# Kernel optimization log

Hardware: AMD Instinct MI355X
Metric: run time of the kernel (lower is better)

## Reference

```python
import jax, jax.numpy as jnp
import numpy as np

B, N, D, OUT = 8, 2048, 128, 128


def setup_inputs() -> dict:
    key = jax.random.key(0)
    k1, k2, kk, kv, ko, kb = jax.random.split(key, 6)
    x1 = jax.random.normal(k1, (B, N, D), dtype=jnp.float32)
    x2 = jax.random.normal(k2, (B, N, D), dtype=jnp.float32)
    # torch Linear weight layout: [out_features, in_features]; xavier_normal std
    std_k = np.sqrt(2.0 / (D + D))
    Wk = jax.random.normal(kk, (D, D), dtype=jnp.float32) * std_k
    Wv = jax.random.normal(kv, (D, D), dtype=jnp.float32) * std_k
    std_o = np.sqrt(1.0 / D)
    Wo = jax.random.uniform(ko, (OUT, D), dtype=jnp.float32, minval=-std_o, maxval=std_o)
    bo = jax.random.uniform(kb, (OUT,), dtype=jnp.float32, minval=-std_o, maxval=std_o)
    return {"x1": x1, "x2": x2, "Wk": Wk, "Wv": Wv, "Wo": Wo, "bo": bo}


def reference(x1, x2, Wk, Wv, Wo, bo):
    # key projections (no bias)
    h1 = jnp.einsum('bnd,kd->bnk', x1, Wk)  # [B,N1,D]
    h2 = jnp.einsum('bmd,kd->bmk', x2, Wk)  # [B,N2,D]
    e12 = jnp.einsum('bnk,bmk->bnm', h1, h2)  # [B,N1,N2]
    e21 = jnp.einsum('bmk,bnk->bmn', h2, h1)  # [B,N2,N1]
    # NOTE: original uses Softmax(dim=1), i.e. over the QUERY axis — faithful here.
    a12 = jax.nn.softmax(e12, axis=1)
    a21 = jax.nn.softmax(e21, axis=1)
    v2 = jnp.einsum('bmd,kd->bmk', x2, Wv)
    v1 = jnp.einsum('bnd,kd->bnk', x1, Wv)
    n12 = jnp.einsum('bnm,bmk->bnk', a12, v2)  # [B,N1,D]
    n21 = jnp.einsum('bmn,bnk->bmk', a21, v1)  # [B,N2,D]
    msg1 = jax.nn.leaky_relu(jnp.einsum('bnk,ok->bno', n12, Wo) + bo, 0.01)
    msg2 = jax.nn.leaky_relu(jnp.einsum('bmk,ok->bmo', n21, Wo) + bo, 0.01)
    return (msg1, msg2)
```

## Files before the change

### kernel.cpp

```cpp
#include <hip/hip_runtime.h>
#include <hip/hip_bf16.h>

#define B_ 8
#define N_ 2048
#define D_ 128
#define CFIX 95.0f

typedef __attribute__((ext_vector_type(8))) _Float16 half8;
typedef __attribute__((ext_vector_type(8))) unsigned short ushort8;
typedef __attribute__((ext_vector_type(4))) float floatx4;
typedef __attribute__((ext_vector_type(16))) float floatx16;

__device__ __forceinline__ unsigned short f2h(float f) {
    _Float16 h = (_Float16)f;
    union { _Float16 h; unsigned short u; } v; v.h = h;
    return v.u;
}
__device__ __forceinline__ ushort4 f2h4(float4 f) {
    ushort4 u; u.x = f2h(f.x); u.y = f2h(f.y); u.z = f2h(f.z); u.w = f2h(f.w);
    return u;
}
__device__ __forceinline__ half8 mk_half8(unsigned int a, unsigned int b,
                                          unsigned int c, unsigned int d) {
    union { unsigned int u[4]; half8 h; } v;
    v.u[0] = a; v.u[1] = b; v.u[2] = c; v.u[3] = d;
    return v.h;
}
__device__ __forceinline__ void plswap(unsigned int &x, unsigned int &y, int hi) {
    unsigned int sx = (unsigned int)__shfl_xor((int)x, 32, 64);
    unsigned int sy = (unsigned int)__shfl_xor((int)y, 32, 64);
    x = hi ? sy : x;
    y = hi ? y : sx;
}

__global__ __launch_bounds__(256)
void proj_kernel(const float* __restrict__ x1, const float* __restrict__ x2,
                 const float* __restrict__ Wk, const float* __restrict__ Wv,
                 unsigned short* __restrict__ h1, unsigned short* __restrict__ h2,
                 unsigned short* __restrict__ v1t, unsigned short* __restrict__ v2t,
                 float* __restrict__ sums)
{
    __shared__ unsigned short Xs[64][136];
    __shared__ unsigned short Ws[128][136];
    const int which = blockIdx.y;
    const float* x = (which & 1) ? x2 : x1;
    const float* W = (which & 2) ? Wv : Wk;
    const int rowbase = blockIdx.x * 64;
    const int t = threadIdx.x;

    {
        int base = (blockIdx.y * 256 + blockIdx.x) * 32;
        if (t < 32) sums[base + t] = 0.0f;
    }

    for (int it = 0; it < 8; ++it) {
        int idx = t + 256 * it;
        int r = idx >> 5, c = (idx & 31) * 4;
        float4 f = *(const float4*)(x + (size_t)(rowbase + r) * 128 + c);
        *(ushort4*)&Xs[r][c] = f2h4(f);
    }
    for (int it = 0; it < 16; ++it) {
        int idx = t + 256 * it;
        int r = idx >> 5, c = (idx & 31) * 4;
        float4 f = *(const float4*)(W + (size_t)r * 128 + c);
        *(ushort4*)&Ws[r][c] = f2h4(f);
    }
    __syncthreads();

    const int lane = t & 63, wave = t >> 6, l15 = lane & 15, quad = lane >> 4;
    half8 a[4];
    for (int ks = 0; ks < 4; ++ks)
        a[ks] = *(const half8*)&Xs[wave * 16 + l15][ks * 32 + quad * 8];
    __syncthreads();

    if (which < 2) {
        unsigned short* out = which ? h2 : h1;
        for (int c = 0; c < 8; ++c) {
            floatx4 acc = {0.f, 0.f, 0.f, 0.f};
            for (int ks = 0; ks < 4; ++ks) {
                half8 b = *(const half8*)&Ws[c * 16 + l15][ks * 32 + quad * 8];
                acc = __builtin_amdgcn_mfma_f32_16x16x32_f16(a[ks], b, acc, 0, 0, 0);
            }
            int col = c * 16 + l15;
            for (int r = 0; r < 4; ++r)
                Xs[wave * 16 + quad * 4 + r][col] = f2h(acc[r]);
        }
        __syncthreads();
        for (int i = 0; i < 4; ++i) {
            int idx = t + 256 * i;
            int r = idx >> 4, c8 = idx & 15;
            ushort8 v = *(const ushort8*)&Xs[r][c8 * 8];
            *(ushort8*)(out + (size_t)(rowbase + r) * 128 + c8 * 8) = v;
        }
    } else {
        unsigned short* vt = (which == 2) ? v1t : v2t;
        unsigned short (*Xt)[68] = (unsigned short (*)[68])&Xs[0][0];
        for (int c = 0; c < 8; ++c) {
            floatx4 acc = {0.f, 0.f, 0.f, 0.f};
            for (int ks = 0; ks < 4; ++ks) {
                half8 b = *(const half8*)&Ws[c * 16 + l15][ks * 32 + quad * 8];
                acc = __builtin_amdgcn_mfma_f32_16x16x32_f16(a[ks], b, acc, 0, 0, 0);
            }
            int col = c * 16 + l15;
            for (int r = 0; r < 4; ++r)
                Xt[col][wave * 16 + quad * 4 + r] = f2h(acc[r]);
        }
        __syncthreads();
        const int bb = rowbase >> 11;
        const int n0 = rowbase & (N_ - 1);
        for (int i = 0; i < 8; ++i) {
            int idx = t + 256 * i;
            int d = idx >> 4, q4 = idx & 15;
            ushort4 v = *(const ushort4*)&Xt[d][q4 * 4];
            *(ushort4*)(vt + ((size_t)bb * 128 + d) * N_ + n0 + q4 * 4) = v;
        }
    }
}

__global__ __launch_bounds__(512, 2)
void stats_kernel(const unsigned short* __restrict__ h1g, const unsigned short* __restrict__ h2g,
                  float* __restrict__ rsum, float* __restrict__ csum)
{
    __shared__ __align__(16) unsigned short Ks[2][2][64][136];

    const int bid = blockIdx.x;
    const int b = bid & 7;
    const int qblk = (bid >> 3) & 15;
    const int dir = bid >> 7;
    const int qbase = qblk * 128;

    const unsigned short* Q = (dir ? h2g : h1g) + (size_t)b * N_ * 128;
    const unsigned short* K = (dir ? h1g : h2g) + (size_t)b * N_ * 128;
    float* outp = (dir ? csum : rsum) + (size_t)b * N_;

    const int t = threadIdx.x;
    const int lane = t & 63, wave = t >> 6;
    const int l31 = lane & 31, h = lane >> 5;
    const int qt = wave & 3, j = wave >> 2;

    half8 qf[8];
    #pragma unroll
    for (int ds = 0; ds < 8; ++ds)
        qf[ds] = *(const half8*)(Q + (size_t)(qbase + qt * 32 + l31) * 128 + ds * 16 + h * 8);

    int krow[2], kc8[2];
    #pragma unroll
    for (int s2 = 0; s2 < 2; ++s2) {
        int idx = t + 512 * s2;
        krow[s2] = idx >> 4; kc8[s2] = idx & 15;
    }
    half8 kreg[2][2];
    #pragma unroll
    for (int jj = 0; jj < 2; ++jj)
        #pragma unroll
        for (int s2 = 0; s2 < 2; ++s2)
            kreg[jj][s2] = *(const half8*)(K + (size_t)(jj * 1024 + krow[s2]) * 128 + kc8[s2] * 8);
    #pragma unroll
    for (int jj = 0; jj < 2; ++jj)
        #pragma unroll
        for (int s2 = 0; s2 < 2; ++s2)
            *(half8*)&Ks[0][jj][krow[s2]][kc8[s2] * 8] = kreg[jj][s2];
    #pragma unroll
    for (int jj = 0; jj < 2; ++jj)
        #pragma unroll
        for (int s2 = 0; s2 < 2; ++s2)
            kreg[jj][s2] = *(const half8*)(K + (size_t)(jj * 1024 + 64 + krow[s2]) * 128 + kc8[s2] * 8);
    __syncthreads();

    float racc = 0.0f;

    for (int kt = 0; kt < 16; ++kt) {
        const int cb = kt & 1;
        #pragma unroll
        for (int jj = 0; jj < 2; ++jj)
            #pragma unroll
            for (int s2 = 0; s2 < 2; ++s2)
                *(half8*)&Ks[cb ^ 1][jj][krow[s2]][kc8[s2] * 8] = kreg[jj][s2];
        int ktp = (kt + 2 < 16) ? kt + 2 : 15;
        #pragma unroll
        for (int jj = 0; jj < 2; ++jj)
            #pragma unroll
            for (int s2 = 0; s2 < 2; ++s2)
                kreg[jj][s2] = *(const half8*)(K + (size_t)(jj * 1024 + ktp * 64 + krow[s2]) * 128 + kc8[s2] * 8);

        #pragma unroll
        for (int ks = 0; ks < 2; ++ks) {
            floatx16 acc;
            #pragma unroll
            for (int r = 0; r < 16; ++r) acc[r] = -CFIX;
            #pragma unroll
            for (int ds = 0; ds < 8; ++ds) {
                half8 kf = *(const half8*)&Ks[cb][j][ks * 32 + l31][ds * 16 + h * 8];
                acc = __builtin_amdgcn_mfma_f32_32x32x16_f16(kf, qf[ds], acc, 0, 0, 0);
            }
            float e[16];
            #pragma unroll
            for (int r = 0; r < 16; ++r) e[r] = __expf(acc[r]);
            #pragma unroll
            for (int st = 8; st > 0; st >>= 1)
                #pragma unroll
                for (int r = 0; r < st; ++r) e[r] += e[r + st];
            racc += e[0];
        }
        __syncthreads();
    }

    racc += __shfl_xor(racc, 32, 64);
    if (h == 0)
        atomicAdd(&outp[qbase + qt * 32 + l31], racc);
}

__global__ __launch_bounds__(512)
void log_kernel(float* __restrict__ sums, const float* __restrict__ Wo,
                unsigned short* __restrict__ wo16)
{
    int i = blockIdx.x * 1024 + threadIdx.x * 2;
    float2 v = *(float2*)(sums + i);
    v.x = -(CFIX + __logf(v.x));
    v.y = -(CFIX + __logf(v.y));
    *(float2*)(sums + i) = v;
    if (blockIdx.x < 16) {
        float2 w = *(const float2*)(Wo + i);
        unsigned int pk = (unsigned int)f2h(w.x) | ((unsigned int)f2h(w.y) << 16);
        *(unsigned int*)(wo16 + i) = pk;
    }
}

__global__ __launch_bounds__(512, 2)
void attn_kernel(const unsigned short* __restrict__ h1g, const unsigned short* __restrict__ h2g,
                 const unsigned short* __restrict__ v1tg, const unsigned short* __restrict__ v2tg,
                 const float* __restrict__ rsumL, const float* __restrict__ csumL,
                 const unsigned short* __restrict__ wo16, const float* __restrict__ bo,
                 float* __restrict__ outp, int zbase)
{
    __shared__ __align__(16) unsigned short Ks[2][2][64][136];
    __shared__ __align__(16) unsigned short Vs[2][2][128][72];

    const int bid = blockIdx.x;
    const int b = bid & 7;
    const int qblk = (bid >> 3) & 15;
    const int dir = (bid >> 7) + zbase;
    const int qbase = qblk * 128;

    const unsigned short* Q  = (dir ? h2g : h1g) + (size_t)b * N_ * 128;
    const unsigned short* K  = (dir ? h1g : h2g) + (size_t)b * N_ * 128;
    const unsigned short* VT = (dir ? v1tg : v2tg) + (size_t)b * 128 * N_;
    const float* SL = (dir ? rsumL : csumL) + (size_t)b * N_;
    float* outbase = outp + (dir ? (size_t)B_ * N_ * 128 : 0);

    const int t = threadIdx.x;
    const int lane = t & 63, wave = t >> 6;
    const int l31 = lane & 31, h = lane >> 5;
    const int qt = wave & 3, j = wave >> 2;

    half8 qf[8];
    #pragma unroll
    for (int ds = 0; ds < 8; ++ds)
        qf[ds] = *(const half8*)(Q + (size_t)(qbase + qt * 32 + l31) * 128 + ds * 16 + h * 8);

    int krow[2], kc8[2], vd[2], vc8[2];
    #pragma unroll
    for (int s2 = 0; s2 < 2; ++s2) {
        int idx = t + 512 * s2;
        krow[s2] = idx >> 4; kc8[s2] = idx & 15;
        vd[s2]   = idx >> 3; vc8[s2] = idx & 7;
    }
    half8 kreg[2][2], vreg[2][2];
    #pragma unroll
    for (int jj = 0; jj < 2; ++jj)
        #pragma unroll
        for (int s2 = 0; s2 < 2; ++s2) {
            kreg[jj][s2] = *(const half8*)(K + (size_t)(jj * 1024 + krow[s2]) * 128 + kc8[s2] * 8);
            vreg[jj][s2] = *(const half8*)(VT + (size_t)vd[s2] * N_ + jj * 1024 + vc8[s2] * 8);
        }
    #pragma unroll
    for (int jj = 0; jj < 2; ++jj)
        #pragma unroll
        for (int s2 = 0; s2 < 2; ++s2) {
            *(half8*)&Ks[0][jj][krow[s2]][kc8[s2] * 8] = kreg[jj][s2];
            *(half8*)&Vs[0][jj][vd[s2]][vc8[s2] * 8]   = vreg[jj][s2];
        }
    #pragma unroll
    for (int jj = 0; jj < 2; ++jj)
        #pragma unroll
        for (int s2 = 0; s2 < 2; ++s2) {
            kreg[jj][s2] = *(const half8*)(K + (size_t)(jj * 1024 + 64 + krow[s2]) * 128 + kc8[s2] * 8);
            vreg[jj][s2] = *(const half8*)(VT + (size_t)vd[s2] * N_ + jj * 1024 + 64 + vc8[s2] * 8);
        }
    __syncthreads();

    floatx16 o0 = {}, o1 = {}, o2 = {}, o3 = {};

    for (int kt = 0; kt < 16; ++kt) {
        const int cb = kt & 1;
        #pragma unroll
        for (int jj = 0; jj < 2; ++jj)
            #pragma unroll
            for (int s2 = 0; s2 < 2; ++s2) {
                *(half8*)&Ks[cb ^ 1][jj][krow[s2]][kc8[s2] * 8] = kreg[jj][s2];
                *(half8*)&Vs[cb ^ 1][jj][vd[s2]][vc8[s2] * 8]   = vreg[jj][s2];
            }
        int ktp = (kt + 2 < 16) ? kt + 2 : 15;
        #pragma unroll
        for (int jj = 0; jj < 2; ++jj)
            #pragma unroll
            for (int s2 = 0; s2 < 2; ++s2) {
                kreg[jj][s2] = *(const half8*)(K + (size_t)(jj * 1024 + ktp * 64 + krow[s2]) * 128 + kc8[s2] * 8);
                vreg[jj][s2] = *(const half8*)(VT + (size_t)vd[s2] * N_ + jj * 1024 + ktp * 64 + vc8[s2] * 8);
            }
        #pragma unroll
        for (int ks = 0; ks < 2; ++ks) {
            const int kb = j * 1024 + kt * 64 + ks * 32;
            float4 L0 = *(const float4*)(SL + kb + 4 * h);
            float4 L1 = *(const float4*)(SL + kb + 4 * h + 8);
            float4 L2 = *(const float4*)(SL + kb + 4 * h + 16);
            float4 L3 = *(const float4*)(SL + kb + 4 * h + 24);
            floatx16 acc;
            acc[0] = L0.x; acc[1] = L0.y; acc[2]  = L0.z; acc[3]  = L0.w;
            acc[4] = L1.x; acc[5] = L1.y; acc[6]  = L1.z; acc[7]  = L1.w;
            acc[8] = L2.x; acc[9] = L2.y; acc[10] = L2.z; acc[11] = L2.w;
            acc[12] = L3.x; acc[13] = L3.y; acc[14] = L3.z; acc[15] = L3.w;
            #pragma unroll
            for (int ds = 0; ds < 8; ++ds) {
                half8 kf = *(const half8*)&Ks[cb][j][ks * 32 + l31][ds * 16 + h * 8];
                acc = __builtin_amdgcn_mfma_f32_32x32x16_f16(kf, qf[ds], acc, 0, 0, 0);
            }
            unsigned int c[8];
            #pragma unroll
            for (int p = 0; p < 8; ++p) {
                unsigned int lo  = f2h(__expf(acc[2 * p]));
                unsigned int hi2 = f2h(__expf(acc[2 * p + 1]));
                c[p] = lo | (hi2 << 16);
            }
            plswap(c[0], c[2], h);
            plswap(c[1], c[3], h);
            plswap(c[4], c[6], h);
            plswap(c[5], c[7], h);
            half8 pa0 = mk_half8(c[0], c[1], c[2], c[3]);
            half8 pa1 = mk_half8(c[4], c[5], c[6], c[7]);
            {
                half8 vb;
                vb = *(const half8*)&Vs[cb][j][0 * 32 + l31][ks * 32 + h * 8];
                o0 = __builtin_amdgcn_mfma_f32_32x32x16_f16(pa0, vb, o0, 0, 0, 0);
                vb = *(const half8*)&Vs[cb][j][0 * 32 + l31][ks * 32 + 16 + h * 8];
                o0 = __builtin_amdgcn_mfma_f32_32x32x16_f16(pa1, vb, o0, 0, 0, 0);
                vb = *(const half8*)&Vs[cb][j][1 * 32 + l31][ks * 32 + h * 8];
                o1 = __builtin_amdgcn_mfma_f32_32x32x16_f16(pa0, vb, o1, 0, 0, 0);
                vb = *(const half8*)&Vs[cb][j][1 * 32 + l31][ks * 32 + 16 + h * 8];
                o1 = __builtin_amdgcn_mfma_f32_32x32x16_f16(pa1, vb, o1, 0, 0, 0);
                vb = *(const half8*)&Vs[cb][j][2 * 32 + l31][ks * 32 + h * 8];
                o2 = __builtin_amdgcn_mfma_f32_32x32x16_f16(pa0, vb, o2, 0, 0, 0);
                vb = *(const half8*)&Vs[cb][j][2 * 32 + l31][ks * 32 + 16 + h * 8];
                o2 = __builtin_amdgcn_mfma_f32_32x32x16_f16(pa1, vb, o2, 0, 0, 0);
                vb = *(const half8*)&Vs[cb][j][3 * 32 + l31][ks * 32 + h * 8];
                o3 = __builtin_amdgcn_mfma_f32_32x32x16_f16(pa0, vb, o3, 0, 0, 0);
                vb = *(const half8*)&Vs[cb][j][3 * 32 + l31][ks * 32 + 16 + h * 8];
                o3 = __builtin_amdgcn_mfma_f32_32x32x16_f16(pa1, vb, o3, 0, 0, 0);
            }
        }
        __syncthreads();
    }

    float (*Rbuf)[32][128] = (float (*)[32][128])&Ks[0][0][0][0];
    unsigned short (*Nsq)[32][136] = (unsigned short (*)[32][136])&Vs[0][0][0][0];
    if (j == 1) {
        #pragma unroll
        for (int r = 0; r < 16; ++r) {
            int row = (r & 3) + 8 * (r >> 2) + 4 * h;
            Rbuf[qt][row][0 * 32 + l31] = o0[r];
            Rbuf[qt][row][1 * 32 + l31] = o1[r];
            Rbuf[qt][row][2 * 32 + l31] = o2[r];
            Rbuf[qt][row][3 * 32 + l31] = o3[r];
        }
    }
    __syncthreads();
    if (j == 0) {
        #pragma unroll
        for (int r = 0; r < 16; ++r) {
            int row = (r & 3) + 8 * (r >> 2) + 4 * h;
            Nsq[qt][row][0 * 32 + l31] = f2h(o0[r] + Rbuf[qt][row][0 * 32 + l31]);
            Nsq[qt][row][1 * 32 + l31] = f2h(o1[r] + Rbuf[qt][row][1 * 32 + l31]);
            Nsq[qt][row][2 * 32 + l31] = f2h(o2[r] + Rbuf[qt][row][2 * 32 + l31]);
            Nsq[qt][row][3 * 32 + l31] = f2h(o3[r] + Rbuf[qt][row][3 * 32 + l31]);
        }
    }
    __syncthreads();
    #pragma unroll
    for (int oc = 0; oc < 2; ++oc) {
        const int ob = j * 64 + oc * 32;
        floatx16 acc2 = {};
        #pragma unroll
        for (int ds = 0; ds < 8; ++ds) {
            half8 na = *(const half8*)&Nsq[qt][l31][ds * 16 + h * 8];
            half8 wb = *(const half8*)(wo16 + (size_t)(ob + l31) * 128 + ds * 16 + h * 8);
            acc2 = __builtin_amdgcn_mfma_f32_32x32x16_f16(na, wb, acc2, 0, 0, 0);
        }
        float bias = bo[ob + l31];
        #pragma unroll
        for (int r = 0; r < 16; ++r) {
            int row = (r & 3) + 8 * (r >> 2) + 4 * h;
            float mv = acc2[r] + bias;
            mv = (mv >= 0.0f) ? mv : 0.01f * mv;
            outbase[(size_t)(b * N_ + qbase + qt * 32 + row) * 128 + ob + l31] = mv;
        }
    }
}

extern "C" void kernel_launch(void* const* d_in, const int* in_sizes, int n_in,
                              void* d_out, int out_size, void* d_ws, size_t ws_size,
                              hipStream_t stream)
{
    const float* x1 = (const float*)d_in[0];
    const float* x2 = (const float*)d_in[1];
    const float* Wk = (const float*)d_in[2];
    const float* Wv = (const float*)d_in[3];
    const float* Wo = (const float*)d_in[4];
    const float* bo = (const float*)d_in[5];
    float* out = (float*)d_out;

    const size_t nrow = (size_t)B_ * N_;
    unsigned short* h1  = (unsigned short*)d_ws;
    unsigned short* h2  = h1 + nrow * 128;
    unsigned short* v1t = h2 + nrow * 128;
    const size_t need = 4 * nrow * 128 * sizeof(unsigned short)
                      + 2 * nrow * sizeof(float) + (size_t)128 * 128 * 2;
    const bool fits = ws_size >= need;

    unsigned short* v2t;
    float* rsum;
    if (fits) {
        v2t = v1t + nrow * 128;
        rsum = (float*)(v2t + nrow * 128);
    } else {
        v2t = (unsigned short*)(out + nrow * 128);
        rsum = (float*)(v1t + nrow * 128);
    }
    float* csum = rsum + nrow;
    unsigned short* wo16 = (unsigned short*)(csum + nrow);

    proj_kernel<<<dim3(256, 4), 256, 0, stream>>>(x1, x2, Wk, Wv, h1, h2, v1t, v2t, rsum);
    stats_kernel<<<dim3(256), 512, 0, stream>>>(h1, h2, rsum, csum);
    log_kernel<<<dim3(32), 512, 0, stream>>>(rsum, Wo, wo16);
    if (fits) {
        attn_kernel<<<dim3(256), 512, 0, stream>>>(h1, h2, v1t, v2t, rsum, csum,
                                                   wo16, bo, out, 0);
    } else {
        attn_kernel<<<dim3(128), 512, 0, stream>>>(h1, h2, v1t, v2t, rsum, csum,
                                                   wo16, bo, out, 0);
        attn_kernel<<<dim3(128), 512, 0, stream>>>(h1, h2, v1t, v2t, rsum, csum,
                                                   wo16, bo, out, 1);
    }
}
```

Baseline: 153.7 us.

## Split key dimension across four wave groups with 1024-thread blocks

Blocks in the stats and attention kernels grow from 512 to 1024 threads, and the key range is split four ways instead of two. Each wave group now streams 32-key tiles per iteration rather than 64, with LDS tiles re-laid out to match. The aim is more waves in flight to hide MFMA, exp and LDS latency. In exchange, partial outputs need two extra serialized Rbuf accumulation passes. The (1024,4) launch bound also caps registers tightly and may cause spills, while the roughly 150KB of LDS still limits each CU to one block.

```diff
diff --git a/kernel.cpp b/kernel.cpp
--- a/kernel.cpp
+++ b/kernel.cpp
@@ -31,6 +31,22 @@
     unsigned int sy = (unsigned int)__shfl_xor((int)y, 32, 64);
     x = hi ? sy : x;
     y = hi ? y : sx;
+}
+__device__ __forceinline__ void pack_pa(const floatx16& acc, int h,
+                                        half8& pa0, half8& pa1) {
+    unsigned int c[8];
+    #pragma unroll
+    for (int p = 0; p < 8; ++p) {
+        unsigned int lo  = f2h(__expf(acc[2 * p]));
+        unsigned int hi2 = f2h(__expf(acc[2 * p + 1]));
+        c[p] = lo | (hi2 << 16);
+    }
+    plswap(c[0], c[2], h);
+    plswap(c[1], c[3], h);
+    plswap(c[4], c[6], h);
+    plswap(c[5], c[7], h);
+    pa0 = mk_half8(c[0], c[1], c[2], c[3]);
+    pa1 = mk_half8(c[4], c[5], c[6], c[7]);
 }
 
 __global__ __launch_bounds__(256)
@@ -117,11 +133,11 @@
     }
 }
 
-__global__ __launch_bounds__(512, 2)
+__global__ __launch_bounds__(1024, 4)
 void stats_kernel(const unsigned short* __restrict__ h1g, const unsigned short* __restrict__ h2g,
                   float* __restrict__ rsum, float* __restrict__ csum)
 {
-    __shared__ __align__(16) unsigned short Ks[2][2][64][136];
+    __shared__ __align__(16) unsigned short Ks[2][4][32][136];
 
     const int bid = blockIdx.x;
     const int b = bid & 7;
@@ -143,28 +159,22 @@
     for (int ds = 0; ds < 8; ++ds)
         qf[ds] = *(const half8*)(Q + (size_t)(qbase + qt * 32 + l31) * 128 + ds * 16 + h * 8);
 
-    int krow[2], kc8[2];
+    int kjj[2], krow[2], kc8[2];
     #pragma unroll
     for (int s2 = 0; s2 < 2; ++s2) {
-        int idx = t + 512 * s2;
-        krow[s2] = idx >> 4; kc8[s2] = idx & 15;
-    }
-    half8 kreg[2][2];
-    #pragma unroll
-    for (int jj = 0; jj < 2; ++jj)
-        #pragma unroll
-        for (int s2 = 0; s2 < 2; ++s2)
-            kreg[jj][s2] = *(const half8*)(K + (size_t)(jj * 1024 + krow[s2]) * 128 + kc8[s2] * 8);
-    #pragma unroll
-    for (int jj = 0; jj < 2; ++jj)
-        #pragma unroll
-        for (int s2 = 0; s2 < 2; ++s2)
-            *(half8*)&Ks[0][jj][krow[s2]][kc8[s2] * 8] = kreg[jj][s2];
-    #pragma unroll
-    for (int jj = 0; jj < 2; ++jj)
-        #pragma unroll
-        for (int s2 = 0; s2 < 2; ++s2)
-            kreg[jj][s2] = *(const half8*)(K + (size_t)(jj * 1024 + 64 + krow[s2]) * 128 + kc8[s2] * 8);
+        int idx = t + 1024 * s2;
+        kjj[s2] = idx >> 9; krow[s2] = (idx >> 4) & 31; kc8[s2] = idx & 15;
+    }
+    half8 kreg[2];
+    #pragma unroll
+    for (int s2 = 0; s2 < 2; ++s2)
+        kreg[s2] = *(const half8*)(K + (size_t)(kjj[s2] * 512 + krow[s2]) * 128 + kc8[s2] * 8);
+    #pragma unroll
+    for (int s2 = 0; s2 < 2; ++s2)
+        *(half8*)&Ks[0][kjj[s2]][krow[s2]][kc8[s2] * 8] = kreg[s2];
+    #pragma unroll
+    for (int s2 = 0; s2 < 2; ++s2)
+        kreg[s2] = *(const half8*)(K + (size_t)(kjj[s2] * 512 + 32 + krow[s2]) * 128 + kc8[s2] * 8);
     __syncthreads();
 
     float racc = 0.0f;
@@ -172,36 +182,29 @@
     for (int kt = 0; kt < 16; ++kt) {
         const int cb = kt & 1;
         #pragma unroll
-        for (int jj = 0; jj < 2; ++jj)
+        for (int s2 = 0; s2 < 2; ++s2)
+            *(half8*)&Ks[cb ^ 1][kjj[s2]][krow[s2]][kc8[s2] * 8] = kreg[s2];
+        int ktp = (kt + 2 < 16) ? kt + 2 : 15;
+        #pragma unroll
+        for (int s2 = 0; s2 < 2; ++s2)
+            kreg[s2] = *(const half8*)(K + (size_t)(kjj[s2] * 512 + ktp * 32 + krow[s2]) * 128 + kc8[s2] * 8);
+
+        floatx16 acc;
+        #pragma unroll
+        for (int r = 0; r < 16; ++r) acc[r] = -CFIX;
+        #pragma unroll
+        for (int ds = 0; ds < 8; ++ds) {
+            half8 kf = *(const half8*)&Ks[cb][j][l31][ds * 16 + h * 8];
+            acc = __builtin_amdgcn_mfma_f32_32x32x16_f16(kf, qf[ds], acc, 0, 0, 0);
+        }
+        float e[16];
+        #pragma unroll
+        for (int r = 0; r < 16; ++r) e[r] = __expf(acc[r]);
+        #pragma unroll
+        for (int st = 8; st > 0; st >>= 1)
             #pragma unroll
-            for (int s2 = 0; s2 < 2; ++s2)
-                *(half8*)&Ks[cb ^ 1][jj][krow[s2]][kc8[s2] * 8] = kreg[jj][s2];
-        int ktp = (kt + 2 < 16) ? kt + 2 : 15;
-        #pragma unroll
-        for (int jj = 0; jj < 2; ++jj)
-            #pragma unroll
-            for (int s2 = 0; s2 < 2; ++s2)
-                kreg[jj][s2] = *(const half8*)(K + (size_t)(jj * 1024 + ktp * 64 + krow[s2]) * 128 + kc8[s2] * 8);
-
-        #pragma unroll
-        for (int ks = 0; ks < 2; ++ks) {
-            floatx16 acc;
-            #pragma unroll
-            for (int r = 0; r < 16; ++r) acc[r] = -CFIX;
-            #pragma unroll
-            for (int ds = 0; ds < 8; ++ds) {
-                half8 kf = *(const half8*)&Ks[cb][j][ks * 32 + l31][ds * 16 + h * 8];
-                acc = __builtin_amdgcn_mfma_f32_32x32x16_f16(kf, qf[ds], acc, 0, 0, 0);
-            }
-            float e[16];
-            #pragma unroll
-            for (int r = 0; r < 16; ++r) e[r] = __expf(acc[r]);
-            #pragma unroll
-            for (int st = 8; st > 0; st >>= 1)
-                #pragma unroll
-                for (int r = 0; r < st; ++r) e[r] += e[r + st];
-            racc += e[0];
-        }
+            for (int r = 0; r < st; ++r) e[r] += e[r + st];
+        racc += e[0];
         __syncthreads();
     }
 
@@ -226,15 +229,15 @@
     }
 }
 
-__global__ __launch_bounds__(512, 2)
+__global__ __launch_bounds__(1024, 4)
 void attn_kernel(const unsigned short* __restrict__ h1g, const unsigned short* __restrict__ h2g,
                  const unsigned short* __restrict__ v1tg, const unsigned short* __restrict__ v2tg,
                  const float* __restrict__ rsumL, const float* __restrict__ csumL,
                  const unsigned short* __restrict__ wo16, const float* __restrict__ bo,
                  float* __restrict__ outp, int zbase)
 {
-    __shared__ __align__(16) unsigned short Ks[2][2][64][136];
-    __shared__ __align__(16) unsigned short Vs[2][2][128][72];
+    __shared__ __align__(16) unsigned short Ks[2][4][32][136];
+    __shared__ __align__(16) unsigned short Vs[2][4][128][40];
 
     const int bid = blockIdx.x;
     const int b = bid & 7;
@@ -258,35 +261,29 @@
     for (int ds = 0; ds < 8; ++ds)
         qf[ds] = *(const half8*)(Q + (size_t)(qbase + qt * 32 + l31) * 128 + ds * 16 + h * 8);
 
-    int krow[2], kc8[2], vd[2], vc8[2];
+    int kjj[2], krow[2], kc8[2], vjj[2], vd[2], vc8[2];
     #pragma unroll
     for (int s2 = 0; s2 < 2; ++s2) {
-        int idx = t + 512 * s2;
-        krow[s2] = idx >> 4; kc8[s2] = idx & 15;
-        vd[s2]   = idx >> 3; vc8[s2] = idx & 7;
-    }
-    half8 kreg[2][2], vreg[2][2];
-    #pragma unroll
-    for (int jj = 0; jj < 2; ++jj)
-        #pragma unroll
-        for (int s2 = 0; s2 < 2; ++s2) {
-            kreg[jj][s2] = *(const half8*)(K + (size_t)(jj * 1024 + krow[s2]) * 128 + kc8[s2] * 8);
-            vreg[jj][s2] = *(const half8*)(VT + (size_t)vd[s2] * N_ + jj * 1024 + vc8[s2] * 8);
-        }
-    #pragma unroll
-    for (int jj = 0; jj < 2; ++jj)
-        #pragma unroll
-        for (int s2 = 0; s2 < 2; ++s2) {
-            *(half8*)&Ks[0][jj][krow[s2]][kc8[s2] * 8] = kreg[jj][s2];
-            *(half8*)&Vs[0][jj][vd[s2]][vc8[s2] * 8]   = vreg[jj][s2];
-        }
-    #pragma unroll
-    for (int jj = 0; jj < 2; ++jj)
-        #pragma unroll
-        for (int s2 = 0; s2 < 2; ++s2) {
-            kreg[jj][s2] = *(const half8*)(K + (size_t)(jj * 1024 + 64 + krow[s2]) * 128 + kc8[s2] * 8);
-            vreg[jj][s2] = *(const half8*)(VT + (size_t)vd[s2] * N_ + jj * 1024 + 64 + vc8[s2] * 8);
-        }
+        int idx = t + 1024 * s2;
+        kjj[s2] = idx >> 9; krow[s2] = (idx >> 4) & 31; kc8[s2] = idx & 15;
+        vjj[s2] = idx >> 9; vd[s2]   = (idx >> 2) & 127; vc8[s2] = idx & 3;
+    }
+    half8 kreg[2], vreg[2];
+    #pragma unroll
+    for (int s2 = 0; s2 < 2; ++s2) {
+        kreg[s2] = *(const half8*)(K + (size_t)(kjj[s2] * 512 + krow[s2]) * 128 + kc8[s2] * 8);
+        vreg[s2] = *(const half8*)(VT + (size_t)vd[s2] * N_ + vjj[s2] * 512 + vc8[s2] * 8);
+    }
+    #pragma unroll
+    for (int s2 = 0; s2 < 2; ++s2) {
+        *(half8*)&Ks[0][kjj[s2]][krow[s2]][kc8[s2] * 8] = kreg[s2];
+        *(half8*)&Vs[0][vjj[s2]][vd[s2]][vc8[s2] * 8]   = vreg[s2];
+    }
+    #pragma unroll
+    for (int s2 = 0; s2 < 2; ++s2) {
+        kreg[s2] = *(const half8*)(K + (size_t)(kjj[s2] * 512 + 32 + krow[s2]) * 128 + kc8[s2] * 8);
+        vreg[s2] = *(const half8*)(VT + (size_t)vd[s2] * N_ + vjj[s2] * 512 + 32 + vc8[s2] * 8);
+    }
     __syncthreads();
 
     floatx16 o0 = {}, o1 = {}, o2 = {}, o3 = {};
@@ -294,69 +291,54 @@
     for (int kt = 0; kt < 16; ++kt) {
         const int cb = kt & 1;
         #pragma unroll
-        for (int jj = 0; jj < 2; ++jj)
-            #pragma unroll
-            for (int s2 = 0; s2 < 2; ++s2) {
-                *(half8*)&Ks[cb ^ 1][jj][krow[s2]][kc8[s2] * 8] = kreg[jj][s2];
-                *(half8*)&Vs[cb ^ 1][jj][vd[s2]][vc8[s2] * 8]   = vreg[jj][s2];
-            }
+        for (int s2 = 0; s2 < 2; ++s2) {
+            *(half8*)&Ks[cb ^ 1][kjj[s2]][krow[s2]][kc8[s2] * 8] = kreg[s2];
+            *(half8*)&Vs[cb ^ 1][vjj[s2]][vd[s2]][vc8[s2] * 8]   = vreg[s2];
+        }
         int ktp = (kt + 2 < 16) ? kt + 2 : 15;
         #pragma unroll
-        for (int jj = 0; jj < 2; ++jj)
-            #pragma unroll
-            for (int s2 = 0; s2 < 2; ++s2) {
-                kreg[jj][s2] = *(const half8*)(K + (size_t)(jj * 1024 + ktp * 64 + krow[s2]) * 128 + kc8[s2] * 8);
-                vreg[jj][s2] = *(const half8*)(VT + (size_t)vd[s2] * N_ + jj * 1024 + ktp * 64 + vc8[s2] * 8);
-            }
-        #pragma unroll
-        for (int ks = 0; ks < 2; ++ks) {
-            const int kb = j * 1024 + kt * 64 + ks * 32;
+        for (int s2 = 0; s2 < 2; ++s2) {
+            kreg[s2] = *(const half8*)(K + (size_t)(kjj[s2] * 512 + ktp * 32 + krow[s2]) * 128 + kc8[s2] * 8);
+            vreg[s2] = *(const half8*)(VT + (size_t)vd[s2] * N_ + vjj[s2] * 512 + ktp * 32 + vc8[s2] * 8);
+        }
+
+        const int kb = j * 512 + kt * 32;
+        floatx16 acc;
+        {
             float4 L0 = *(const float4*)(SL + kb + 4 * h);
             float4 L1 = *(const float4*)(SL + kb + 4 * h + 8);
             float4 L2 = *(const float4*)(SL + kb + 4 * h + 16);
             float4 L3 = *(const float4*)(SL + kb + 4 * h + 24);
-            floatx16 acc;
             acc[0] = L0.x; acc[1] = L0.y; acc[2]  = L0.z; acc[3]  = L0.w;
             acc[4] = L1.x; acc[5] = L1.y; acc[6]  = L1.z; acc[7]  = L1.w;
             acc[8] = L2.x; acc[9] = L2.y; acc[10] = L2.z; acc[11] = L2.w;
             acc[12] = L3.x; acc[13] = L3.y; acc[14] = L3.z; acc[15] = L3.w;
-            #pragma unroll
-            for (int ds = 0; ds < 8; ++ds) {
-                half8 kf = *(const half8*)&Ks[cb][j][ks * 32 + l31][ds * 16 + h * 8];
-                acc = __builtin_amdgcn_mfma_f32_32x32x16_f16(kf, qf[ds], acc, 0, 0, 0);
-            }
-            unsigned int c[8];
-            #pragma unroll
-            for (int p = 0; p < 8; ++p) {
-                unsigned int lo  = f2h(__expf(acc[2 * p]));
-                unsigned int hi2 = f2h(__expf(acc[2 * p + 1]));
-                c[p] = lo | (hi2 << 16);
-            }
-            plswap(c[0], c[2], h);
-            plswap(c[1], c[3], h);
-            plswap(c[4], c[6], h);
-            plswap(c[5], c[7], h);
-            half8 pa0 = mk_half8(c[0], c[1], c[2], c[3]);
-            half8 pa1 = mk_half8(c[4], c[5], c[6], c[7]);
-            {
-                half8 vb;
-                vb = *(const half8*)&Vs[cb][j][0 * 32 + l31][ks * 32 + h * 8];
-                o0 = __builtin_amdgcn_mfma_f32_32x32x16_f16(pa0, vb, o0, 0, 0, 0);
-                vb = *(const half8*)&Vs[cb][j][0 * 32 + l31][ks * 32 + 16 + h * 8];
-                o0 = __builtin_amdgcn_mfma_f32_32x32x16_f16(pa1, vb, o0, 0, 0, 0);
-                vb = *(const half8*)&Vs[cb][j][1 * 32 + l31][ks * 32 + h * 8];
-                o1 = __builtin_amdgcn_mfma_f32_32x32x16_f16(pa0, vb, o1, 0, 0, 0);
-                vb = *(const half8*)&Vs[cb][j][1 * 32 + l31][ks * 32 + 16 + h * 8];
-                o1 = __builtin_amdgcn_mfma_f32_32x32x16_f16(pa1, vb, o1, 0, 0, 0);
-                vb = *(const half8*)&Vs[cb][j][2 * 32 + l31][ks * 32 + h * 8];
-                o2 = __builtin_amdgcn_mfma_f32_32x32x16_f16(pa0, vb, o2, 0, 0, 0);
-                vb = *(const half8*)&Vs[cb][j][2 * 32 + l31][ks * 32 + 16 + h * 8];
-                o2 = __builtin_amdgcn_mfma_f32_32x32x16_f16(pa1, vb, o2, 0, 0, 0);
-                vb = *(const half8*)&Vs[cb][j][3 * 32 + l31][ks * 32 + h * 8];
-                o3 = __builtin_amdgcn_mfma_f32_32x32x16_f16(pa0, vb, o3, 0, 0, 0);
-                vb = *(const half8*)&Vs[cb][j][3 * 32 + l31][ks * 32 + 16 + h * 8];
-                o3 = __builtin_amdgcn_mfma_f32_32x32x16_f16(pa1, vb, o3, 0, 0, 0);
-            }
+        }
+        #pragma unroll
+        for (int ds = 0; ds < 8; ++ds) {
+            half8 kf = *(const half8*)&Ks[cb][j][l31][ds * 16 + h * 8];
+            acc = __builtin_amdgcn_mfma_f32_32x32x16_f16(kf, qf[ds], acc, 0, 0, 0);
+        }
+        half8 pa0, pa1;
+        pack_pa(acc, h, pa0, pa1);
+        {
+            half8 vb;
+            vb = *(const half8*)&Vs[cb][j][0 * 32 + l31][0 + h * 8];
+            o0 = __builtin_amdgcn_mfma_f32_32x32x16_f16(pa0, vb, o0, 0, 0, 0);
+            vb = *(const half8*)&Vs[cb][j][1 * 32 + l31][0 + h * 8];
+            o1 = __builtin_amdgcn_mfma_f32_32x32x16_f16(pa0, vb, o1, 0, 0, 0);
+            vb = *(const half8*)&Vs[cb][j][2 * 32 + l31][0 + h * 8];
+            o2 = __builtin_amdgcn_mfma_f32_32x32x16_f16(pa0, vb, o2, 0, 0, 0);
+            vb = *(const half8*)&Vs[cb][j][3 * 32 + l31][0 + h * 8];
+            o3 = __builtin_amdgcn_mfma_f32_32x32x16_f16(pa0, vb, o3, 0, 0, 0);
+            vb = *(const half8*)&Vs[cb][j][0 * 32 + l31][16 + h * 8];
+            o0 = __builtin_amdgcn_mfma_f32_32x32x16_f16(pa1, vb, o0, 0, 0, 0);
+            vb = *(const half8*)&Vs[cb][j][1 * 32 + l31][16 + h * 8];
+            o1 = __builtin_amdgcn_mfma_f32_32x32x16_f16(pa1, vb, o1, 0, 0, 0);
+            vb = *(const half8*)&Vs[cb][j][2 * 32 + l31][16 + h * 8];
+            o2 = __builtin_amdgcn_mfma_f32_32x32x16_f16(pa1, vb, o2, 0, 0, 0);
+            vb = *(const half8*)&Vs[cb][j][3 * 32 + l31][16 + h * 8];
+            o3 = __builtin_amdgcn_mfma_f32_32x32x16_f16(pa1, vb, o3, 0, 0, 0);
         }
         __syncthreads();
     }
@@ -374,6 +356,28 @@
         }
     }
     __syncthreads();
+    if (j == 2) {
+        #pragma unroll
+        for (int r = 0; r < 16; ++r) {
+            int row = (r & 3) + 8 * (r >> 2) + 4 * h;
+            Rbuf[qt][row][0 * 32 + l31] += o0[r];
+            Rbuf[qt][row][1 * 32 + l31] += o1[r];
+            Rbuf[qt][row][2 * 32 + l31] += o2[r];
+            Rbuf[qt][row][3 * 32 + l31] += o3[r];
+        }
+    }
+    __syncthreads();
+    if (j == 3) {
+        #pragma unroll
+        for (int r = 0; r < 16; ++r) {
+            int row = (r & 3) + 8 * (r >> 2) + 4 * h;
+            Rbuf[qt][row][0 * 32 + l31] += o0[r];
+            Rbuf[qt][row][1 * 32 + l31] += o1[r];
+            Rbuf[qt][row][2 * 32 + l31] += o2[r];
+            Rbuf[qt][row][3 * 32 + l31] += o3[r];
+        }
+    }
+    __syncthreads();
     if (j == 0) {
         #pragma unroll
         for (int r = 0; r < 16; ++r) {
@@ -385,9 +389,8 @@
         }
     }
     __syncthreads();
-    #pragma unroll
-    for (int oc = 0; oc < 2; ++oc) {
-        const int ob = j * 64 + oc * 32;
+    {
+        const int ob = j * 32;
         floatx16 acc2 = {};
         #pragma unroll
         for (int ds = 0; ds < 8; ++ds) {
@@ -439,15 +442,15 @@
     unsigned short* wo16 = (unsigned short*)(csum + nrow);
 
     proj_kernel<<<dim3(256, 4), 256, 0, stream>>>(x1, x2, Wk, Wv, h1, h2, v1t, v2t, rsum);
-    stats_kernel<<<dim3(256), 512, 0, stream>>>(h1, h2, rsum, csum);
+    stats_kernel<<<dim3(256), 1024, 0, stream>>>(h1, h2, rsum, csum);
     log_kernel<<<dim3(32), 512, 0, stream>>>(rsum, Wo, wo16);
     if (fits) {
-        attn_kernel<<<dim3(256), 512, 0, stream>>>(h1, h2, v1t, v2t, rsum, csum,
-                                                   wo16, bo, out, 0);
+        attn_kernel<<<dim3(256), 1024, 0, stream>>>(h1, h2, v1t, v2t, rsum, csum,
+                                                    wo16, bo, out, 0);
     } else {
-        attn_kernel<<<dim3(128), 512, 0, stream>>>(h1, h2, v1t, v2t, rsum, csum,
-                                                   wo16, bo, out, 0);
-        attn_kernel<<<dim3(128), 512, 0, stream>>>(h1, h2, v1t, v2t, rsum, csum,
-                                                   wo16, bo, out, 1);
-    }
-}
+        attn_kernel<<<dim3(128), 1024, 0, stream>>>(h1, h2, v1t, v2t, rsum, csum,
+                                                    wo16, bo, out, 0);
+        attn_kernel<<<dim3(128), 1024, 0, stream>>>(h1, h2, v1t, v2t, rsum, csum,
+                                                    wo16, bo, out, 1);
+    }
+}
```

After: 177.1 us. 1.15x slower.
